# Kernel optimization log

Measured on AMD Instinct MI355X. Metric: run time of the kernel, lower is better.

## Reference

```python
import jax, jax.numpy as jnp
import numpy as np

CH_IN = 256
CA = CH_IN // 8   # attention channels (theta/phi)
CH = CH_IN // 2   # value channels (g)


def _maxpool2(t):
    # 2x2 max pool, stride 2: (B,C,H,W) -> (B,C,H//2,W//2)
    b, c, h, w = t.shape
    return t.reshape(b, c, h // 2, 2, w // 2, 2).max(axis=(3, 5))


def setup_inputs() -> dict:
    key = jax.random.key(0)
    ks = jax.random.split(key, 6)
    B, H, W = 16, 64, 64
    x = jax.random.normal(ks[0], (B, CH_IN, H, W), dtype=jnp.float32)
    # 1x1 conv weights stored as (out_ch, in_ch); spectral_norm is a weight
    # reparameterization, so the forward math is a plain conv with these weights.
    s = 0.05
    w_theta = jax.random.normal(ks[1], (CA, CH_IN), dtype=jnp.float32) * s
    w_phi = jax.random.normal(ks[2], (CA, CH_IN), dtype=jnp.float32) * s
    w_g = jax.random.normal(ks[3], (CH, CH_IN), dtype=jnp.float32) * s
    w_o = jax.random.normal(ks[4], (CH_IN, CH), dtype=jnp.float32) * s
    # gamma is initialized to 0 in the module; use a nonzero value so the
    # attention branch contributes to the output.
    gamma = jnp.asarray(0.5, dtype=jnp.float32)
    return {"x": x, "w_theta": w_theta, "w_phi": w_phi, "w_g": w_g,
            "w_o": w_o, "gamma": gamma}


def reference(x, w_theta, w_phi, w_g, w_o, gamma):
    B, C, H, W = x.shape
    # 1x1 convs as channel contractions
    theta = jnp.einsum('oc,bchw->bohw', w_theta, x)            # (B,CA,H,W)
    phi = _maxpool2(jnp.einsum('oc,bchw->bohw', w_phi, x))     # (B,CA,H/2,W/2)
    g = _maxpool2(jnp.einsum('oc,bchw->bohw', w_g, x))         # (B,CH,H/2,W/2)
    N = H * W
    M = N // 4
    theta = theta.reshape(B, CA, N)
    phi = phi.reshape(B, CA, M)
    g = g.reshape(B, CH, M)
    # beta = softmax(theta^T phi) over keys (no scaling, as in original)
    beta = jax.nn.softmax(jnp.einsum('bcn,bcm->bnm', theta, phi), axis=-1)  # (B,N,M)
    o = jnp.einsum('bcm,bnm->bcn', g, beta).reshape(B, CH, H, W)
    o = jnp.einsum('oc,bchw->bohw', w_o, o)                    # (B,C,H,W)
    return gamma * o + x
```

## Files before the change

### kernel.cpp

```cpp
#include <hip/hip_runtime.h>
#include <hip/hip_bf16.h>

#define NB 16
#define CIN 256
#define CA 32
#define CH 128
#define NN 4096
#define MM 1024

typedef __attribute__((ext_vector_type(8))) short s16x8;
typedef __attribute__((ext_vector_type(4))) float f32x4;

static __device__ __forceinline__ unsigned short f2bf(float x) {
  __hip_bfloat16 h = __float2bfloat16(x);
  return __builtin_bit_cast(unsigned short, h);
}
static __device__ __forceinline__ float bf2f(unsigned short u) {
  unsigned int v = ((unsigned int)u) << 16;
  return __builtin_bit_cast(float, v);
}
static __device__ __forceinline__ unsigned int pk2(float a, float b) {
  return (unsigned)f2bf(a) | ((unsigned)f2bf(b) << 16);
}
static __device__ __forceinline__ void gload_lds16(const void* g, void* s) {
  __builtin_amdgcn_global_load_lds(
      (const __attribute__((address_space(1))) unsigned int*)g,
      (__attribute__((address_space(3))) unsigned int*)s, 16, 0, 0);
}

__global__ __launch_bounds__(256) void k_wcvt(const float* __restrict__ w_theta,
                                              const float* __restrict__ w_phi,
                                              const float* __restrict__ w_g,
                                              const float* __restrict__ w_o,
                                              unsigned short* __restrict__ wcat2,
                                              unsigned short* __restrict__ wo2) {
  const int i = blockIdx.x * 256 + threadIdx.x;
  if (i < 49152) {
    const int row = i >> 8, c = i & 255;
    const float v = (row < 32) ? w_theta[i]
                  : (row < 64) ? w_phi[i - 8192]
                               : w_g[i - 16384];
    const int dst = ((row >> 4) * 8 + (c >> 5)) * 512 +
                    (((c >> 3) & 3) * 16 + (row & 15)) * 8 + (c & 7);
    wcat2[dst] = f2bf(v);
  } else {
    const int w = i - 49152;
    const int c_out = w >> 7, k = w & 127;
    const int dst = (((c_out >> 4) * 16) + ((k >> 5) * 4) + ((k >> 3) & 3)) * 128 +
                    ((c_out & 15) << 3) + (k & 7);
    wo2[dst] = f2bf(w_o[w]);
  }
}

__global__ __launch_bounds__(512) void k_proj(const float* __restrict__ x,
                                              const unsigned short* __restrict__ wcat2,
                                              unsigned short* __restrict__ theta,
                                              unsigned short* __restrict__ phi2,
                                              unsigned short* __restrict__ g2) {
  __shared__ unsigned short lds[192 * 136];
  unsigned short (*xl)[32][132] = reinterpret_cast<unsigned short(*)[32][132]>(lds);
  unsigned short (*ol)[136] = reinterpret_cast<unsigned short(*)[136]>(lds);
  const int b = blockIdx.y;
  const int t = blockIdx.x;
  const int tid = threadIdx.x;
  const int wv = tid >> 6;
  const int l = tid & 63;
  const int grp = l >> 4, col = l & 15;
  const float* xb = x + (size_t)b * CIN * NN;
  auto STAGEX = [&](int buf, int kc) {
#pragma unroll
    for (int s = 0; s < 2; ++s) {
      const int i = tid + s * 512;
      const int cl = i >> 5, nq = i & 31;
      const float4 v = *reinterpret_cast<const float4*>(
          xb + (size_t)(kc * 32 + cl) * NN + t * 128 + nq * 4);
      *reinterpret_cast<uint2*>(&xl[buf][cl][nq * 4]) =
          make_uint2(pk2(v.x, v.y), pk2(v.z, v.w));
    }
  };
  f32x4 acc[12];
#pragma unroll
  for (int r = 0; r < 12; ++r) acc[r] = f32x4{0.f, 0.f, 0.f, 0.f};
  STAGEX(0, 0);
#pragma unroll 1
  for (int kc = 0; kc < 8; ++kc) {
    __syncthreads();
    if (kc < 7) STAGEX((kc + 1) & 1, kc + 1);
    const int cur = kc & 1;
    s16x8 bfrag;
#pragma unroll
    for (int j = 0; j < 8; ++j)
      bfrag[j] = (short)xl[cur][grp * 8 + j][wv * 16 + col];
#pragma unroll
    for (int r = 0; r < 12; ++r) {
      const s16x8 af = *reinterpret_cast<const s16x8*>(
          wcat2 + (size_t)(r * 8 + kc) * 512 + l * 8);
      acc[r] = __builtin_amdgcn_mfma_f32_16x16x32_bf16(af, bfrag, acc[r], 0, 0, 0);
    }
  }
  __syncthreads();
#pragma unroll
  for (int r = 0; r < 12; ++r)
#pragma unroll
    for (int q = 0; q < 4; ++q)
      ol[r * 16 + grp * 4 + q][wv * 16 + col] = f2bf(acc[r][q]);
  __syncthreads();
  unsigned short* thb = theta + (size_t)b * NN * CA;
  for (int i = tid; i < 128 * 16; i += 512) {
    const int n = i >> 4, cp = (i & 15) << 1;
    const unsigned int v = (unsigned)ol[cp][n] | ((unsigned)ol[cp + 1][n] << 16);
    *reinterpret_cast<unsigned int*>(thb + (size_t)(t * 128 + n) * CA + cp) = v;
  }
  unsigned short* phb2 = phi2 + (size_t)b * MM * CA;
  for (int i = tid; i < 32 * 32; i += 512) {
    const int ca = i & 31, mx = i >> 5;
    const float v = fmaxf(
        fmaxf(bf2f(ol[32 + ca][2 * mx]), bf2f(ol[32 + ca][2 * mx + 1])),
        fmaxf(bf2f(ol[32 + ca][64 + 2 * mx]), bf2f(ol[32 + ca][64 + 2 * mx + 1])));
    const int m = t * 32 + mx;
    phb2[(m >> 4) * 512 + (ca >> 3) * 128 + (m & 15) * 8 + (ca & 7)] = f2bf(v);
  }
  unsigned short* gb2 = g2 + (size_t)b * CH * MM;
  for (int i = tid; i < 128 * 32; i += 512) {
    const int mx = i & 31, c = i >> 5;
    const float v = fmaxf(
        fmaxf(bf2f(ol[64 + c][2 * mx]), bf2f(ol[64 + c][2 * mx + 1])),
        fmaxf(bf2f(ol[64 + c][64 + 2 * mx]), bf2f(ol[64 + c][64 + 2 * mx + 1])));
    const int pg = (mx & 15) >> 2;
    const int pj = (mx & 3) | ((mx >> 4) << 2);
    gb2[(size_t)(t * 8 + (c >> 4)) * 512 + pg * 128 + (c & 15) * 8 + pj] = f2bf(v);
  }
}

__global__ __launch_bounds__(512, 4) void k_attn_out(
    const unsigned short* __restrict__ theta, const unsigned short* __restrict__ phi2,
    const unsigned short* __restrict__ g2, const unsigned short* __restrict__ wo2,
    const float* __restrict__ x, const float* __restrict__ gammap,
    float* __restrict__ out) {
  __shared__ __align__(16) unsigned short kv[2][10240];
  const int b = blockIdx.y;
  const int tid = threadIdx.x;
  const int wv = tid >> 6;
  const int l = tid & 63;
  const int grp = l >> 4, col = l & 15;
  const int n0 = blockIdx.x * 128 + wv * 16;
  const unsigned short* thb = theta + (size_t)b * NN * CA;
  const unsigned short* ph2b = phi2 + (size_t)b * MM * CA;
  const unsigned short* gb2 = g2 + (size_t)b * CH * MM;
  const s16x8 qf = *reinterpret_cast<const s16x8*>(thb + (size_t)(n0 + col) * CA + grp * 8);

  auto STAGE = [&](int buf, int tile) {
    const int mc = tile * 64;
    const unsigned short* ksrc = ph2b + (mc >> 4) * 512;
    const unsigned short* vsrc = gb2 + (size_t)(mc >> 5) * 4096;
#pragma unroll
    for (int q = 0; q < 3; ++q) {
      const int i = wv + q * 8;
      if (i < 20) {
        const unsigned short* src = (i < 4) ? (ksrc + i * 512) : (vsrc + (size_t)(i - 4) * 512);
        gload_lds16(src + (size_t)l * 8, &kv[buf][i * 512]);
      }
    }
  };

  f32x4 oa[8];
#pragma unroll
  for (int t = 0; t < 8; ++t) oa[t] = f32x4{0.f, 0.f, 0.f, 0.f};
  float m0 = -INFINITY, l0 = 0.f;
  const f32x4 z4 = {0.f, 0.f, 0.f, 0.f};

  STAGE(0, 0);
  __syncthreads();
#pragma unroll 1
  for (int it = 0; it < 16; ++it) {
    const int cur = it & 1;
    if (it < 15) STAGE(cur ^ 1, it + 1);
    const unsigned short* kb = &kv[cur][0];
    const unsigned short* vb = &kv[cur][2048];
    const int fo = grp * 128 + col * 8;
    const s16x8 kf0 = *reinterpret_cast<const s16x8*>(kb + 0 * 512 + fo);
    const s16x8 kf1 = *reinterpret_cast<const s16x8*>(kb + 1 * 512 + fo);
    const s16x8 kf2 = *reinterpret_cast<const s16x8*>(kb + 2 * 512 + fo);
    const s16x8 kf3 = *reinterpret_cast<const s16x8*>(kb + 3 * 512 + fo);
    f32x4 s0 = __builtin_amdgcn_mfma_f32_16x16x32_bf16(kf0, qf, z4, 0, 0, 0);
    f32x4 s1 = __builtin_amdgcn_mfma_f32_16x16x32_bf16(kf1, qf, z4, 0, 0, 0);
    f32x4 s2 = __builtin_amdgcn_mfma_f32_16x16x32_bf16(kf2, qf, z4, 0, 0, 0);
    f32x4 s3 = __builtin_amdgcn_mfma_f32_16x16x32_bf16(kf3, qf, z4, 0, 0, 0);
    float cm = -INFINITY;
#pragma unroll
    for (int r = 0; r < 4; ++r)
      cm = fmaxf(cm, fmaxf(fmaxf(s0[r], s1[r]), fmaxf(s2[r], s3[r])));
    cm = fmaxf(cm, __shfl_xor(cm, 16));
    cm = fmaxf(cm, __shfl_xor(cm, 32));
    if (!__all(cm <= m0 + 8.f)) {
      const float mn = fmaxf(m0, cm);
      const float sc = __expf(m0 - mn);
      l0 *= sc;
#pragma unroll
      for (int t = 0; t < 8; ++t) {
#pragma unroll
        for (int r = 0; r < 4; ++r) oa[t][r] *= sc;
      }
      m0 = mn;
    }
    float p0[4], p1[4], p2[4], p3[4];
    float cs = 0.f;
#pragma unroll
    for (int r = 0; r < 4; ++r) {
      p0[r] = __expf(s0[r] - m0);
      p1[r] = __expf(s1[r] - m0);
      p2[r] = __expf(s2[r] - m0);
      p3[r] = __expf(s3[r] - m0);
      cs += (p0[r] + p1[r]) + (p2[r] + p3[r]);
    }
    cs += __shfl_xor(cs, 16);
    cs += __shfl_xor(cs, 32);
    l0 += cs;
    const uint4 ua = make_uint4(pk2(p0[0], p0[1]), pk2(p0[2], p0[3]),
                                pk2(p1[0], p1[1]), pk2(p1[2], p1[3]));
    const uint4 ub = make_uint4(pk2(p2[0], p2[1]), pk2(p2[2], p2[3]),
                                pk2(p3[0], p3[1]), pk2(p3[2], p3[3]));
    const s16x8 pfA = __builtin_bit_cast(s16x8, ua);
    const s16x8 pfB = __builtin_bit_cast(s16x8, ub);
#pragma unroll
    for (int t = 0; t < 8; ++t) {
      const s16x8 vfA = *reinterpret_cast<const s16x8*>(vb + t * 512 + fo);
      const s16x8 vfB = *reinterpret_cast<const s16x8*>(vb + 4096 + t * 512 + fo);
      oa[t] = __builtin_amdgcn_mfma_f32_16x16x32_bf16(vfA, pfA, oa[t], 0, 0, 0);
      oa[t] = __builtin_amdgcn_mfma_f32_16x16x32_bf16(vfB, pfB, oa[t], 0, 0, 0);
    }
    __syncthreads();
  }
  unsigned short* obw = &kv[0][0] + (size_t)wv * (16 * 136);
  const float ri = 1.f / l0;
#pragma unroll
  for (int t = 0; t < 8; ++t) {
    *reinterpret_cast<uint2*>(obw + col * 136 + t * 16 + grp * 4) =
        make_uint2(pk2(oa[t][0] * ri, oa[t][1] * ri),
                   pk2(oa[t][2] * ri, oa[t][3] * ri));
  }
  s16x8 of[4];
#pragma unroll
  for (int ks = 0; ks < 4; ++ks)
    of[ks] = *reinterpret_cast<const s16x8*>(obw + col * 136 + ks * 32 + grp * 8);
  const float gamma = gammap[0];
  const float* xb2 = x + (size_t)b * CIN * NN;
  float* outb = out + (size_t)b * CIN * NN;
#pragma unroll 1
  for (int t2 = 0; t2 < 16; ++t2) {
    f32x4 a2 = {0.f, 0.f, 0.f, 0.f};
#pragma unroll
    for (int ks = 0; ks < 4; ++ks) {
      const s16x8 wf = *reinterpret_cast<const s16x8*>(
          wo2 + (size_t)(t2 * 16 + ks * 4 + grp) * 128 + col * 8);
      a2 = __builtin_amdgcn_mfma_f32_16x16x32_bf16(wf, of[ks], a2, 0, 0, 0);
    }
#pragma unroll
    for (int r = 0; r < 4; ++r) {
      const size_t idx = (size_t)(t2 * 16 + grp * 4 + r) * NN + n0 + col;
      outb[idx] = fmaf(gamma, a2[r], xb2[idx]);
    }
  }
}

extern "C" void kernel_launch(void* const* d_in, const int* in_sizes, int n_in,
                              void* d_out, int out_size, void* d_ws, size_t ws_size,
                              hipStream_t stream) {
  const float* x = (const float*)d_in[0];
  const float* w_theta = (const float*)d_in[1];
  const float* w_phi = (const float*)d_in[2];
  const float* w_g = (const float*)d_in[3];
  const float* w_o = (const float*)d_in[4];
  const float* gamma = (const float*)d_in[5];
  float* out = (float*)d_out;
  char* ws = (char*)d_ws;
  unsigned short* theta = (unsigned short*)(ws + 0);
  unsigned short* phi2 = (unsigned short*)(ws + 4194304);
  unsigned short* g2 = (unsigned short*)(ws + 5242880);
  unsigned short* wo2 = (unsigned short*)(ws + 9437184);
  unsigned short* wcat2 = (unsigned short*)(ws + 9502720);

  k_wcvt<<<dim3(320), 256, 0, stream>>>(w_theta, w_phi, w_g, w_o, wcat2, wo2);
  k_proj<<<dim3(NN / 128, NB), 512, 0, stream>>>(x, wcat2, theta, phi2, g2);
  k_attn_out<<<dim3(NN / 128, NB), 512, 0, stream>>>(theta, phi2, g2, wo2, x, gamma, out);
}
```

Before: 78.56 us.

## Stage projection input per-wave with register prefetch; defer softmax sum reduction

In the projection kernel, each wave now loads and converts its own 16-column slice of x into a private LDS region, prefetching the next channel chunk into registers. This removes the block-wide __syncthreads and double-buffered shared staging from the K loop. In the attention kernel, the cross-lane shuffle reduction of the softmax row sum moves out of the loop to a single reduction after it, because rescaling is uniform across lanes. The per-wave x loads are narrower (32-byte segments per row) and the wave writes then reads its own LDS slice without an explicit barrier, relying on in-wave ordering.

```diff
diff --git a/kernel.cpp b/kernel.cpp
--- a/kernel.cpp
+++ b/kernel.cpp
@@ -58,7 +58,7 @@
                                               unsigned short* __restrict__ phi2,
                                               unsigned short* __restrict__ g2) {
   __shared__ unsigned short lds[192 * 136];
-  unsigned short (*xl)[32][132] = reinterpret_cast<unsigned short(*)[32][132]>(lds);
+  unsigned short (*xlw)[32][24] = reinterpret_cast<unsigned short(*)[32][24]>(lds);
   unsigned short (*ol)[136] = reinterpret_cast<unsigned short(*)[136]>(lds);
   const int b = blockIdx.y;
   const int t = blockIdx.x;
@@ -66,44 +66,43 @@
   const int wv = tid >> 6;
   const int l = tid & 63;
   const int grp = l >> 4, col = l & 15;
+  const int n0 = t * 128 + wv * 16;
+  const int r = l >> 1, h = l & 1;
   const float* xb = x + (size_t)b * CIN * NN;
-  auto STAGEX = [&](int buf, int kc) {
-#pragma unroll
-    for (int s = 0; s < 2; ++s) {
-      const int i = tid + s * 512;
-      const int cl = i >> 5, nq = i & 31;
-      const float4 v = *reinterpret_cast<const float4*>(
-          xb + (size_t)(kc * 32 + cl) * NN + t * 128 + nq * 4);
-      *reinterpret_cast<uint2*>(&xl[buf][cl][nq * 4]) =
-          make_uint2(pk2(v.x, v.y), pk2(v.z, v.w));
-    }
-  };
   f32x4 acc[12];
 #pragma unroll
-  for (int r = 0; r < 12; ++r) acc[r] = f32x4{0.f, 0.f, 0.f, 0.f};
-  STAGEX(0, 0);
+  for (int q = 0; q < 12; ++q) acc[q] = f32x4{0.f, 0.f, 0.f, 0.f};
+  float4 a0 = *reinterpret_cast<const float4*>(xb + (size_t)r * NN + n0 + h * 8);
+  float4 a1 = *reinterpret_cast<const float4*>(xb + (size_t)r * NN + n0 + h * 8 + 4);
 #pragma unroll 1
   for (int kc = 0; kc < 8; ++kc) {
-    __syncthreads();
-    if (kc < 7) STAGEX((kc + 1) & 1, kc + 1);
-    const int cur = kc & 1;
+    float4 b0, b1;
+    if (kc < 7) {
+      const float* src = xb + (size_t)((kc + 1) * 32 + r) * NN + n0 + h * 8;
+      b0 = *reinterpret_cast<const float4*>(src);
+      b1 = *reinterpret_cast<const float4*>(src + 4);
+    }
+    *reinterpret_cast<uint4*>(&xlw[wv][r][h * 8]) =
+        make_uint4(pk2(a0.x, a0.y), pk2(a0.z, a0.w), pk2(a1.x, a1.y), pk2(a1.z, a1.w));
     s16x8 bfrag;
 #pragma unroll
     for (int j = 0; j < 8; ++j)
-      bfrag[j] = (short)xl[cur][grp * 8 + j][wv * 16 + col];
-#pragma unroll
-    for (int r = 0; r < 12; ++r) {
+      bfrag[j] = (short)xlw[wv][grp * 8 + j][col];
+#pragma unroll
+    for (int q = 0; q < 12; ++q) {
       const s16x8 af = *reinterpret_cast<const s16x8*>(
-          wcat2 + (size_t)(r * 8 + kc) * 512 + l * 8);
-      acc[r] = __builtin_amdgcn_mfma_f32_16x16x32_bf16(af, bfrag, acc[r], 0, 0, 0);
-    }
+          wcat2 + (size_t)(q * 8 + kc) * 512 + l * 8);
+      acc[q] = __builtin_amdgcn_mfma_f32_16x16x32_bf16(af, bfrag, acc[q], 0, 0, 0);
+    }
+    a0 = b0;
+    a1 = b1;
   }
   __syncthreads();
 #pragma unroll
-  for (int r = 0; r < 12; ++r)
-#pragma unroll
-    for (int q = 0; q < 4; ++q)
-      ol[r * 16 + grp * 4 + q][wv * 16 + col] = f2bf(acc[r][q]);
+  for (int q = 0; q < 12; ++q)
+#pragma unroll
+    for (int p = 0; p < 4; ++p)
+      ol[q * 16 + grp * 4 + p][wv * 16 + col] = f2bf(acc[q][p]);
   __syncthreads();
   unsigned short* thb = theta + (size_t)b * NN * CA;
   for (int i = tid; i < 128 * 16; i += 512) {
@@ -166,7 +165,7 @@
   f32x4 oa[8];
 #pragma unroll
   for (int t = 0; t < 8; ++t) oa[t] = f32x4{0.f, 0.f, 0.f, 0.f};
-  float m0 = -INFINITY, l0 = 0.f;
+  float m0 = -INFINITY, ls = 0.f;
   const f32x4 z4 = {0.f, 0.f, 0.f, 0.f};
 
   STAGE(0, 0);
@@ -195,7 +194,7 @@
     if (!__all(cm <= m0 + 8.f)) {
       const float mn = fmaxf(m0, cm);
       const float sc = __expf(m0 - mn);
-      l0 *= sc;
+      ls *= sc;
 #pragma unroll
       for (int t = 0; t < 8; ++t) {
 #pragma unroll
@@ -213,9 +212,7 @@
       p3[r] = __expf(s3[r] - m0);
       cs += (p0[r] + p1[r]) + (p2[r] + p3[r]);
     }
-    cs += __shfl_xor(cs, 16);
-    cs += __shfl_xor(cs, 32);
-    l0 += cs;
+    ls += cs;
     const uint4 ua = make_uint4(pk2(p0[0], p0[1]), pk2(p0[2], p0[3]),
                                 pk2(p1[0], p1[1]), pk2(p1[2], p1[3]));
     const uint4 ub = make_uint4(pk2(p2[0], p2[1]), pk2(p2[2], p2[3]),
@@ -231,8 +228,10 @@
     }
     __syncthreads();
   }
+  ls += __shfl_xor(ls, 16);
+  ls += __shfl_xor(ls, 32);
   unsigned short* obw = &kv[0][0] + (size_t)wv * (16 * 136);
-  const float ri = 1.f / l0;
+  const float ri = 1.f / ls;
 #pragma unroll
   for (int t = 0; t < 8; ++t) {
     *reinterpret_cast<uint2*>(obw + col * 136 + t * 16 + grp * 4) =
```

After: 87.40 us. +11.3%, slower.
